# Performance work log

Hardware: AMD Instinct MI355X
Metric: run time of the kernel (lower is better)

## Reference

```python
import jax, jax.numpy as jnp
import numpy as np

NUM_HEADS = 8
BN_EPS = 1e-3


def _conv2d(x, w, padding):
    # x: (B, Cin, H, W), w: (Cout, Cin, kh, kw)
    return jax.lax.conv_general_dilated(
        x, w, window_strides=(1, 1), padding=padding,
        dimension_numbers=("NCHW", "OIHW", "NCHW"))


def setup_inputs() -> dict:
    key = jax.random.key(0)
    ks = jax.random.split(key, 6)
    B, C, H, W = 8, 256, 64, 64
    L, D = 80, 256
    return {
        "img_feat": jax.random.normal(ks[0], (B, C, H, W), jnp.float32),
        "text_feats": jax.random.normal(ks[1], (B, L, D), jnp.float32),
        "proj_w": jax.random.normal(ks[2], (D, C, 1, 1), jnp.float32) * (1.0 / np.sqrt(C)),
        "proj_b": jax.random.normal(ks[3], (D,), jnp.float32) * 0.02,
        "attn_bias": jnp.zeros((NUM_HEADS,), jnp.float32),
        "scale": jnp.ones((1, NUM_HEADS, 1, 1), jnp.float32),
        "conv_w": jax.random.normal(ks[4], (C, C, 3, 3), jnp.float32) * (1.0 / np.sqrt(9 * C)),
        "bn_gamma": jnp.ones((C,), jnp.float32),
        "bn_beta": jnp.zeros((C,), jnp.float32),
        "bn_mean": jnp.zeros((C,), jnp.float32),
        "bn_var": jnp.ones((C,), jnp.float32),
    }


def reference(img_feat, text_feats, proj_w, proj_b, attn_bias, scale,
              conv_w, bn_gamma, bn_beta, bn_mean, bn_var):
    B, C, H, W = img_feat.shape
    hc = proj_w.shape[0] // NUM_HEADS  # head_channels

    # img_proj: 1x1 conv + bias -> (B, heads, hc, H, W)
    i_feat = _conv2d(img_feat, proj_w, "VALID") + proj_b[None, :, None, None]
    i_feat = i_feat.reshape(B, NUM_HEADS, hc, H, W)

    # text: (B, L, heads, hc)
    t_feat = text_feats.reshape(B, -1, NUM_HEADS, hc)

    # attn score over text tokens, then max over tokens
    attn = jnp.einsum("bmchw,bnmc->bmhwn", i_feat, t_feat)  # (B, heads, H, W, L)
    attn = jnp.max(attn, axis=-1)
    attn = attn / jnp.sqrt(jnp.asarray(hc, img_feat.dtype))
    attn = attn + attn_bias[None, :, None, None]
    attn = jax.nn.sigmoid(attn) * scale  # (B, heads, H, W)

    # project_conv: 3x3 conv (no bias) + BN (inference), no activation
    x = _conv2d(img_feat, conv_w, [(1, 1), (1, 1)])
    inv = bn_gamma / jnp.sqrt(bn_var + BN_EPS)
    x = x * inv[None, :, None, None] + (bn_beta - bn_mean * inv)[None, :, None, None]

    # gate per head and flatten back to (B, C, H, W)
    x = x.reshape(B, NUM_HEADS, -1, H, W) * attn[:, :, None]
    return x.reshape(B, -1, H, W)
```

## Files before the change

kernel.cpp:

```cpp
#include <hip/hip_runtime.h>
#include <cmath>

constexpr int kB  = 8;
constexpr int kC  = 256;
constexpr int kH  = 64;
constexpr int kW  = 64;
constexpr int kP  = kH * kW;
constexpr int kL  = 80;
constexpr int kD  = 256;
constexpr int kNH = 8;

typedef short  short8 __attribute__((ext_vector_type(8)));
typedef float  f32x4  __attribute__((ext_vector_type(4)));
typedef unsigned short ushort_t;

__device__ __forceinline__ ushort_t f2bf(float f) {
  unsigned u = __builtin_bit_cast(unsigned, f);
  u += 0x7fffu + ((u >> 16) & 1u);
  return (ushort_t)(u >> 16);
}

__device__ __forceinline__ short8 pack8(float4 a, float4 b) {
  ushort_t tmp[8] = {f2bf(a.x), f2bf(a.y), f2bf(a.z), f2bf(a.w),
                     f2bf(b.x), f2bf(b.y), f2bf(b.z), f2bf(b.w)};
  return *(short8*)tmp;
}

__global__ __launch_bounds__(256) void prep_kernel(
    const float* __restrict__ cw, const float* __restrict__ pw,
    ushort_t* __restrict__ w2, ushort_t* __restrict__ pwb) {
  const int n_w2 = 9 * kC * kC;
  int idx = blockIdx.x * 256 + threadIdx.x;
  if (idx < n_w2) {
    int ci  = idx & 255;
    int co  = (idx >> 8) & 255;
    int tap = idx >> 16;
    w2[idx] = f2bf(cw[(co * kC + ci) * 9 + tap]);
  } else if (idx < n_w2 + kD * kC) {
    int r = idx - n_w2;
    pwb[r] = f2bf(pw[r]);
  }
}

__global__ __launch_bounds__(256) void attn_mfma_kernel(
    const float* __restrict__ img,
    const float* __restrict__ text,
    const ushort_t* __restrict__ pwb,
    const float* __restrict__ pb,
    const float* __restrict__ bias,
    const float* __restrict__ scale,
    ushort_t* __restrict__ imgT,
    float* __restrict__ attn_out) {
  __shared__ ushort_t SB[64 * 40];
  __shared__ ushort_t SI[64 * 264];

  const int b    = blockIdx.x;
  const int p0   = blockIdx.y * 64;
  const int t    = threadIdx.x;
  const int w    = t >> 6;
  const int lane = t & 63;
  const int lr   = lane & 15;
  const int lq   = lane >> 4;
  const int d0   = w * 64;

  const float* imgb  = img  + (size_t)b * kC * kP + p0;
  ushort_t*    imgTb = imgT + (size_t)(b * kP + p0) * kC;

  f32x4 acc[4][4] = {};

  for (int kc = 0; kc < kC; kc += 32) {
    __syncthreads();
#pragma unroll
    for (int i = 0; i < 4; i++) {
      int e = t + i * 256;
      int px = e & 63, ci2 = (e >> 6) * 2;
      ushort_t u[2];
      u[0] = f2bf(imgb[(size_t)(kc + ci2)     * kP + px]);
      u[1] = f2bf(imgb[(size_t)(kc + ci2 + 1) * kP + px]);
      *(unsigned*)&SB[px * 40 + ci2] = *(unsigned*)u;
    }
    __syncthreads();
    {
      int px = t >> 2, cq = (t & 3) * 8;
      *(uint4*)&imgTb[(size_t)px * kC + kc + cq] = *(const uint4*)&SB[px * 40 + cq];
    }
    short8 afr[4], bfr[4];
#pragma unroll
    for (int mt = 0; mt < 4; mt++)
      afr[mt] = *(const short8*)&pwb[(size_t)(d0 + mt * 16 + lr) * kC + kc + lq * 8];
#pragma unroll
    for (int nt = 0; nt < 4; nt++)
      bfr[nt] = *(const short8*)&SB[(nt * 16 + lr) * 40 + lq * 8];
#pragma unroll
    for (int mt = 0; mt < 4; mt++)
#pragma unroll
      for (int nt = 0; nt < 4; nt++)
        acc[mt][nt] = __builtin_amdgcn_mfma_f32_16x16x32_bf16(afr[mt], bfr[nt], acc[mt][nt], 0, 0, 0);
  }

#pragma unroll
  for (int mt = 0; mt < 4; mt++) {
    float4 pb4 = *(const float4*)(pb + d0 + mt * 16 + lq * 4);
#pragma unroll
    for (int nt = 0; nt < 4; nt++) {
      ushort_t v[4];
      v[0] = f2bf(acc[mt][nt][0] + pb4.x);
      v[1] = f2bf(acc[mt][nt][1] + pb4.y);
      v[2] = f2bf(acc[mt][nt][2] + pb4.z);
      v[3] = f2bf(acc[mt][nt][3] + pb4.w);
      *(ulonglong1*)&SI[(nt * 16 + lr) * 264 + d0 + mt * 16 + lq * 4] = *(ulonglong1*)v;
    }
  }

  const float* textb = text + (size_t)b * kL * kD;
#pragma unroll
  for (int lh = 0; lh < 2; lh++) {
    const int h = 2 * w + lh;
    const float bh = bias[h], sh = scale[h];
    short8 atok[5];
#pragma unroll
    for (int mt = 0; mt < 5; mt++) {
      const float* p = textb + (size_t)(mt * 16 + lr) * kD + h * 32 + lq * 8;
      atok[mt] = pack8(*(const float4*)p, *(const float4*)(p + 4));
    }
#pragma unroll
    for (int nt = 0; nt < 4; nt++) {
      short8 bfr2 = *(const short8*)&SI[(nt * 16 + lr) * 264 + h * 32 + lq * 8];
      float vmax = -3.4e38f;
#pragma unroll
      for (int mt = 0; mt < 5; mt++) {
        f32x4 z = {};
        f32x4 d = __builtin_amdgcn_mfma_f32_16x16x32_bf16(atok[mt], bfr2, z, 0, 0, 0);
        vmax = fmaxf(vmax, fmaxf(fmaxf(d[0], d[1]), fmaxf(d[2], d[3])));
      }
      vmax = fmaxf(vmax, __shfl_xor(vmax, 16));
      vmax = fmaxf(vmax, __shfl_xor(vmax, 32));
      if (lq == 0) {
        float lg = vmax * 0.17677669529663687f + bh;
        float a  = sh / (1.0f + expf(-lg));
        attn_out[((size_t)(b * kNH + h)) * kP + p0 + nt * 16 + lr] = a;
      }
    }
  }
}

__global__ __launch_bounds__(256) void conv_mfma_kernel(
    const ushort_t* __restrict__ imgT,
    const ushort_t* __restrict__ w2,
    const float* __restrict__ gamma,
    const float* __restrict__ beta,
    const float* __restrict__ mean,
    const float* __restrict__ var,
    const float* __restrict__ attn,
    float* __restrict__ out) {
  __shared__ ushort_t Al[6 * 66 * 40];
  __shared__ ushort_t Wl[9 * 64 * 40];

  const int b   = blockIdx.x;
  const int h0  = blockIdx.y * 4;
  const int co0 = blockIdx.z * 64;
  const int t   = threadIdx.x;
  const int w   = t >> 6;
  const int lane = t & 63;
  const int lr  = lane & 15;
  const int lq  = lane >> 4;

  const ushort_t* imgTb = imgT + (size_t)b * kP * kC;

  f32x4 acc[4][4] = {};

  for (int kc = 0; kc < kC; kc += 32) {
    __syncthreads();
    for (int e = t; e < 6 * 66 * 4; e += 256) {
      int r   = e / 264;
      int rem = e - r * 264;
      int c   = rem >> 2;
      int cq  = (rem & 3) * 8;
      int row = h0 - 1 + r;
      uint4 v = make_uint4(0, 0, 0, 0);
      if (row >= 0 && row < kH && c >= 1 && c <= 64) {
        int px = row * kW + (c - 1);
        v = *(const uint4*)&imgTb[(size_t)px * kC + kc + cq];
      }
      *(uint4*)&Al[(r * 66 + c) * 40 + cq] = v;
    }
    {
      int e = t;
#pragma unroll
      for (int i = 0; i < 9; i++, e += 256) {
        int cq  = (e & 3) * 8;
        int co  = (e >> 2) & 63;
        int tap = e >> 8;
        uint4 v = *(const uint4*)&w2[((size_t)(tap * kC + co0 + co)) * kC + kc + cq];
        *(uint4*)&Wl[(tap * 64 + co) * 40 + cq] = v;
      }
    }
    __syncthreads();

    const int abase = (w * 66 + lr) * 40 + lq * 8;
    const int wbase = lr * 40 + lq * 8;
#pragma unroll
    for (int tap = 0; tap < 9; tap++) {
      const int kh = tap / 3, kw = tap % 3;
      short8 bi[4];
#pragma unroll
      for (int nt = 0; nt < 4; nt++)
        bi[nt] = *(const short8*)&Al[abase + (kh * 66 + kw + nt * 16) * 40];
      short8 aw[4];
#pragma unroll
      for (int mt = 0; mt < 4; mt++)
        aw[mt] = *(const short8*)&Wl[wbase + (tap * 64 + mt * 16) * 40];
#pragma unroll
      for (int mt = 0; mt < 4; mt++)
#pragma unroll
        for (int nt = 0; nt < 4; nt++)
          acc[mt][nt] = __builtin_amdgcn_mfma_f32_16x16x32_bf16(
              aw[mt], bi[nt], acc[mt][nt], 0, 0, 0);
    }
  }

  const int h = h0 + w;
  float* outb = out + (size_t)b * kC * kP + h * kW;
#pragma unroll
  for (int mt = 0; mt < 4; mt++) {
    const int head = (co0 + mt * 16) >> 5;
    const float* arow = attn + ((size_t)(b * kNH + head)) * kP + h * kW;
    float inv_v[4], bb_v[4];
#pragma unroll
    for (int reg = 0; reg < 4; reg++) {
      int co = co0 + mt * 16 + lq * 4 + reg;
      float inv = gamma[co] * rsqrtf(var[co] + 1e-3f);
      inv_v[reg] = inv;
      bb_v[reg]  = beta[co] - mean[co] * inv;
    }
#pragma unroll
    for (int nt = 0; nt < 4; nt++) {
      const int col = nt * 16 + lr;
      const float av = arow[col];
#pragma unroll
      for (int reg = 0; reg < 4; reg++) {
        int co = co0 + mt * 16 + lq * 4 + reg;
        outb[(size_t)co * kP + col] = (acc[mt][nt][reg] * inv_v[reg] + bb_v[reg]) * av;
      }
    }
  }
}

extern "C" void kernel_launch(void* const* d_in, const int* in_sizes, int n_in,
                              void* d_out, int out_size, void* d_ws, size_t ws_size,
                              hipStream_t stream) {
  const float* img   = (const float*)d_in[0];
  const float* text  = (const float*)d_in[1];
  const float* pw    = (const float*)d_in[2];
  const float* pb    = (const float*)d_in[3];
  const float* bias  = (const float*)d_in[4];
  const float* scale = (const float*)d_in[5];
  const float* cw    = (const float*)d_in[6];
  const float* gam   = (const float*)d_in[7];
  const float* bet   = (const float*)d_in[8];
  const float* mea   = (const float*)d_in[9];
  const float* va    = (const float*)d_in[10];
  float* out = (float*)d_out;

  char* ws = (char*)d_ws;
  float*    attn = (float*)ws;
  ushort_t* imgT = (ushort_t*)(ws + (1u << 20));
  ushort_t* w2   = (ushort_t*)(ws + (1u << 20) + (16u << 20));
  ushort_t* pwb  = (ushort_t*)(ws + (1u << 20) + (16u << 20) + 1179648u);

  {
    int n = 9 * kC * kC + kD * kC;
    prep_kernel<<<(n + 255) / 256, 256, 0, stream>>>(cw, pw, w2, pwb);
  }
  {
    dim3 grid(kB, kP / 64);
    attn_mfma_kernel<<<grid, 256, 0, stream>>>(img, text, pwb, pb, bias, scale, imgT, attn);
  }
  {
    dim3 grid(kB, kH / 4, kC / 64);
    conv_mfma_kernel<<<grid, 256, 0, stream>>>(imgT, w2, gam, bet, mea, va, attn, out);
  }
}
```

Before: 159.5 us.

## Load conv tiles directly into LDS with global_load_lds and swizzled weight layout

The conv kernel now fills its LDS tiles with direct global-to-LDS loads (global_load_lds, 16 bytes) instead of loading through registers. To make that work, the prep kernel writes the weights in a pre-tiled, XOR-swizzled layout, and LDS drops its padding, relying on the swizzle to avoid bank conflicts. It also skips MFMA work for kernel rows that fall outside the image and zeroes the halo columns only once. This removes register staging and the per-element address math, but depends on the exact lane-to-LDS layout of the direct loads being correct.

```diff
diff --git a/kernel.cpp b/kernel.cpp
--- a/kernel.cpp
+++ b/kernel.cpp
@@ -26,16 +26,31 @@
   return *(short8*)tmp;
 }
 
+__device__ __forceinline__ void gl_lds16(const void* gp, void* lp) {
+  __builtin_amdgcn_global_load_lds(
+      (const __attribute__((address_space(1))) void*)gp,
+      (__attribute__((address_space(3))) void*)lp,
+      16, 0, 0);
+}
+
 __global__ __launch_bounds__(256) void prep_kernel(
     const float* __restrict__ cw, const float* __restrict__ pw,
-    ushort_t* __restrict__ w2, ushort_t* __restrict__ pwb) {
+    ushort_t* __restrict__ w2s, ushort_t* __restrict__ pwb) {
   const int n_w2 = 9 * kC * kC;
   int idx = blockIdx.x * 256 + threadIdx.x;
   if (idx < n_w2) {
-    int ci  = idx & 255;
-    int co  = (idx >> 8) & 255;
-    int tap = idx >> 16;
-    w2[idx] = f2bf(cw[(co * kC + ci) * 9 + tap]);
+    int j    = idx & 7;
+    int G    = idx >> 3;
+    int s    = G & 3;
+    int co_l = (G >> 2) & 63;
+    int cbt  = G >> 8;
+    int tap  = cbt % 9;
+    int cb   = cbt / 9;
+    int chunk = cb >> 2, cob = cb & 3;
+    int g    = s ^ (co_l & 3);
+    int ci   = chunk * 32 + g * 8 + j;
+    int co   = cob * 64 + co_l;
+    w2s[idx] = f2bf(cw[(co * kC + ci) * 9 + tap]);
   } else if (idx < n_w2 + kD * kC) {
     int r = idx - n_w2;
     pwb[r] = f2bf(pw[r]);
@@ -146,76 +161,81 @@
 
 __global__ __launch_bounds__(256) void conv_mfma_kernel(
     const ushort_t* __restrict__ imgT,
-    const ushort_t* __restrict__ w2,
+    const ushort_t* __restrict__ w2s,
     const float* __restrict__ gamma,
     const float* __restrict__ beta,
     const float* __restrict__ mean,
     const float* __restrict__ var,
     const float* __restrict__ attn,
     float* __restrict__ out) {
-  __shared__ ushort_t Al[6 * 66 * 40];
-  __shared__ ushort_t Wl[9 * 64 * 40];
-
-  const int b   = blockIdx.x;
-  const int h0  = blockIdx.y * 4;
-  const int co0 = blockIdx.z * 64;
-  const int t   = threadIdx.x;
-  const int w   = t >> 6;
+  __shared__ ushort_t Al[6 * 66 * 32];
+  __shared__ ushort_t Wl[9 * 256 * 8];
+
+  const int b    = blockIdx.x;
+  const int h0   = blockIdx.y * 4;
+  const int cob  = blockIdx.z;
+  const int co0  = cob * 64;
+  const int t    = threadIdx.x;
+  const int w    = t >> 6;
   const int lane = t & 63;
-  const int lr  = lane & 15;
-  const int lq  = lane >> 4;
+  const int lr   = lane & 15;
+  const int lq   = lane >> 4;
+
+  if (t < 48) {
+    int r = t >> 3, cc = (t >> 2) & 1, s4 = t & 3;
+    int col = cc ? 65 : 0;
+    *(uint4*)&Al[(r * 66 + col) * 32 + s4 * 8] = make_uint4(0, 0, 0, 0);
+  }
 
   const ushort_t* imgTb = imgT + (size_t)b * kP * kC;
 
   f32x4 acc[4][4] = {};
 
-  for (int kc = 0; kc < kC; kc += 32) {
+  for (int kc8 = 0; kc8 < 8; kc8++) {
+    const int kc = kc8 * 32;
+    const ushort_t* w2sb = w2s + (size_t)(kc8 * 4 + cob) * 9 * 2048;
     __syncthreads();
-    for (int e = t; e < 6 * 66 * 4; e += 256) {
-      int r   = e / 264;
-      int rem = e - r * 264;
-      int c   = rem >> 2;
-      int cq  = (rem & 3) * 8;
-      int row = h0 - 1 + r;
-      uint4 v = make_uint4(0, 0, 0, 0);
-      if (row >= 0 && row < kH && c >= 1 && c <= 64) {
-        int px = row * kW + (c - 1);
-        v = *(const uint4*)&imgTb[(size_t)px * kC + kc + cq];
-      }
-      *(uint4*)&Al[(r * 66 + c) * 40 + cq] = v;
-    }
-    {
-      int e = t;
-#pragma unroll
-      for (int i = 0; i < 9; i++, e += 256) {
-        int cq  = (e & 3) * 8;
-        int co  = (e >> 2) & 63;
-        int tap = e >> 8;
-        uint4 v = *(const uint4*)&w2[((size_t)(tap * kC + co0 + co)) * kC + kc + cq];
-        *(uint4*)&Wl[(tap * 64 + co) * 40 + cq] = v;
+    for (int j = w; j < 60; j += 4) {
+      if (j < 24) {
+        int r = j >> 2, q = j & 3;
+        int rimg = h0 - 1 + r;
+        if (rimg >= 0 && rimg < kH) {
+          int colq = q * 16 + (lane >> 2);
+          int s    = lane & 3;
+          const ushort_t* g = imgTb + ((size_t)(rimg * kW + colq)) * kC + kc + s * 8;
+          gl_lds16(g, &Al[(r * 66 + 1) * 32 + q * 512]);
+        }
+      } else {
+        int jj = j - 24, tap = jj >> 2, q = jj & 3;
+        const ushort_t* g = w2sb + ((size_t)(tap * 256 + q * 64 + lane)) * 8;
+        gl_lds16(g, &Wl[(tap * 256 + q * 64) * 8]);
       }
     }
     __syncthreads();
 
-    const int abase = (w * 66 + lr) * 40 + lq * 8;
-    const int wbase = lr * 40 + lq * 8;
-#pragma unroll
-    for (int tap = 0; tap < 9; tap++) {
-      const int kh = tap / 3, kw = tap % 3;
-      short8 bi[4];
-#pragma unroll
-      for (int nt = 0; nt < 4; nt++)
-        bi[nt] = *(const short8*)&Al[abase + (kh * 66 + kw + nt * 16) * 40];
-      short8 aw[4];
-#pragma unroll
-      for (int mt = 0; mt < 4; mt++)
-        aw[mt] = *(const short8*)&Wl[wbase + (tap * 64 + mt * 16) * 40];
-#pragma unroll
-      for (int mt = 0; mt < 4; mt++)
+#pragma unroll
+    for (int kh = 0; kh < 3; kh++) {
+      const int rimg = h0 + w + kh - 1;
+      if (rimg < 0 || rimg >= kH) continue;
+      const int ar = (w + kh) * 66 * 32;
+#pragma unroll
+      for (int kw = 0; kw < 3; kw++) {
+        const int tap = kh * 3 + kw;
+        short8 bi[4];
 #pragma unroll
         for (int nt = 0; nt < 4; nt++)
-          acc[mt][nt] = __builtin_amdgcn_mfma_f32_16x16x32_bf16(
-              aw[mt], bi[nt], acc[mt][nt], 0, 0, 0);
+          bi[nt] = *(const short8*)&Al[ar + (kw + nt * 16 + lr) * 32 + lq * 8];
+        short8 aw[4];
+#pragma unroll
+        for (int mt = 0; mt < 4; mt++)
+          aw[mt] = *(const short8*)&Wl[(tap * 256 + (mt * 16 + lr) * 4 + (lq ^ (lr & 3))) * 8];
+#pragma unroll
+        for (int mt = 0; mt < 4; mt++)
+#pragma unroll
+          for (int nt = 0; nt < 4; nt++)
+            acc[mt][nt] = __builtin_amdgcn_mfma_f32_16x16x32_bf16(
+                aw[mt], bi[nt], acc[mt][nt], 0, 0, 0);
+      }
     }
   }
 
@@ -265,12 +285,12 @@
   char* ws = (char*)d_ws;
   float*    attn = (float*)ws;
   ushort_t* imgT = (ushort_t*)(ws + (1u << 20));
-  ushort_t* w2   = (ushort_t*)(ws + (1u << 20) + (16u << 20));
+  ushort_t* w2s  = (ushort_t*)(ws + (1u << 20) + (16u << 20));
   ushort_t* pwb  = (ushort_t*)(ws + (1u << 20) + (16u << 20) + 1179648u);
 
   {
     int n = 9 * kC * kC + kD * kC;
-    prep_kernel<<<(n + 255) / 256, 256, 0, stream>>>(cw, pw, w2, pwb);
+    prep_kernel<<<(n + 255) / 256, 256, 0, stream>>>(cw, pw, w2s, pwb);
   }
   {
     dim3 grid(kB, kP / 64);
@@ -278,6 +298,6 @@
   }
   {
     dim3 grid(kB, kH / 4, kC / 64);
-    conv_mfma_kernel<<<grid, 256, 0, stream>>>(imgT, w2, gam, bet, mea, va, attn, out);
-  }
-}
+    conv_mfma_kernel<<<grid, 256, 0, stream>>>(imgT, w2s, gam, bet, mea, va, attn, out);
+  }
+}
```

Measured after the change: 154.7 us. -3.0%, faster.
